# Kernel optimization log

Measured on AMD Instinct MI355X. Metric: run time of the kernel, lower is better.

## Reference

```python
import jax, jax.numpy as jnp
import numpy as np

B, T, OBS = 16, 4095, 128
HID, NH, FF, NL = 256, 8, 1024, 4
DH = HID // NH
ACT = 32
KEPS = 0.001   # performer kernel_epsilon (generalized attention default)
LNEPS = 1e-6   # flax LayerNorm default eps


def setup_inputs() -> dict:
    key = jax.random.key(0)
    ks = list(jax.random.split(key, 16))
    s = 0.02
    r = lambda k, shape: jax.random.normal(k, shape, jnp.float32) * s
    return {
        "hidden_state": jnp.zeros((B, 1, HID), jnp.float32),
        "ins": jax.random.normal(ks[0], (B, T, OBS), jnp.float32),
        "resets": jax.random.randint(ks[1], (B,), 0, 2).astype(bool),
        "emb_W": r(ks[2], (OBS, HID)), "emb_b": jnp.zeros((HID,), jnp.float32),
        "Wq": r(ks[3], (NL, HID, NH, DH)), "bq": jnp.zeros((NL, NH, DH), jnp.float32),
        "Wk": r(ks[4], (NL, HID, NH, DH)), "bk": jnp.zeros((NL, NH, DH), jnp.float32),
        "Wv": r(ks[5], (NL, HID, NH, DH)), "bv": jnp.zeros((NL, NH, DH), jnp.float32),
        "Wo": r(ks[6], (NL, NH, DH, HID)), "bo": jnp.zeros((NL, HID), jnp.float32),
        "ln1_s": jnp.ones((NL, HID), jnp.float32), "ln1_b": jnp.zeros((NL, HID), jnp.float32),
        "W1": r(ks[7], (NL, HID, FF)), "b1": jnp.zeros((NL, FF), jnp.float32),
        "W2": r(ks[8], (NL, FF, HID)), "b2": jnp.zeros((NL, HID), jnp.float32),
        "ln2_s": jnp.ones((NL, HID), jnp.float32), "ln2_b": jnp.zeros((NL, HID), jnp.float32),
        "qp_W": r(ks[9], (HID, ACT)), "qp_b": jnp.zeros((ACT,), jnp.float32),
    }


def layer_norm(x, scale, bias):
    m = x.mean(-1, keepdims=True)
    v = ((x - m) ** 2).mean(-1, keepdims=True)
    return (x - m) * jax.lax.rsqrt(v + LNEPS) * scale + bias


def favor_attention(q, k, v):
    # FAVOR+ generalized attention with deterministic relu features (no random
    # projection, make_fast_generalized_attention defaults), bidirectional,
    # renormalized. q,k,v: [B, L, H, Dh]; feature dim M == Dh.
    qp = jax.nn.relu(q) + KEPS
    kp = jax.nn.relu(k) + KEPS
    kv = jnp.einsum('blhm,blhd->bhmd', kp, v)            # [B,H,M,Dh]
    num = jnp.einsum('blhm,bhmd->blhd', qp, kv)           # [B,L,H,Dh]
    den = jnp.einsum('blhm,bhm->blh', qp, kp.sum(axis=1))  # [B,L,H]
    return num / den[..., None]


def encoder_block(x, Wq, bq, Wk, bk, Wv, bv, Wo, bo, ln1_s, ln1_b, W1, b1, W2, b2, ln2_s, ln2_b):
    q = jnp.einsum('bld,dhm->blhm', x, Wq) + bq
    k = jnp.einsum('bld,dhm->blhm', x, Wk) + bk
    v = jnp.einsum('bld,dhm->blhm', x, Wv) + bv
    a = favor_attention(q, k, v)
    o = jnp.einsum('blhm,hmd->bld', a, Wo) + bo
    x = o + o  # faithful to source: x = attn(x); x = x + dropout(x)
    x = layer_norm(x, ln1_s, ln1_b)
    h = jax.nn.relu(x @ W1 + b1) @ W2 + b2
    h = h + h  # same residual quirk on the FFN branch
    return layer_norm(h, ln2_s, ln2_b)


def reference(hidden_state, ins, resets, emb_W, emb_b, Wq, bq, Wk, bk, Wv, bv, Wo, bo, ln1_s, ln1_b, W1, b1, W2, b2, ln2_s, ln2_b, qp_W, qp_b):
    emb = ins @ emb_W + emb_b                         # [B, T, HID]
    hs = jnp.where(resets[:, None, None], 0.0, hidden_state)
    x = jnp.concatenate([hs, emb], axis=-2)           # [B, 1+T, HID]
    for i in range(NL):
        x = encoder_block(x, Wq[i], bq[i], Wk[i], bk[i], Wv[i], bv[i], Wo[i], bo[i],
                          ln1_s[i], ln1_b[i], W1[i], b1[i], W2[i], b2[i], ln2_s[i], ln2_b[i])
    new_hidden = x[..., 0:1, :]                       # carry token
    q_vals = new_hidden @ qp_W + qp_b                 # [B, 1, ACT]
    return new_hidden, q_vals
```

## Files before the change

### kernel.cpp

```cpp
#include <hip/hip_runtime.h>


typedef unsigned short bf16_t;
typedef __attribute__((ext_vector_type(8))) short short8;
typedef __attribute__((ext_vector_type(4))) float float4v;

#define NB 16
#define LSEQ 4096
#define MROWS (NB * LSEQ)
#define HIDD 256
#define NHEAD 8
#define DHEAD 32
#define FFD 1024
#define NLAY 4
#define KEPS_F 1e-3f
#define LNEPS_F 1e-6f
#define KV_ELEMS (NB * NHEAD * 32 * 33)

__device__ __forceinline__ float b2f(bf16_t h) {
    return __uint_as_float(((unsigned int)h) << 16);
}
__device__ __forceinline__ bf16_t f2b(float f) {
    unsigned int u = __float_as_uint(f);
    u += 0x7fffu + ((u >> 16) & 1u);
    return (bf16_t)(u >> 16);
}

#define GLOAD_LDS16(g, l)                                                     \
    __builtin_amdgcn_global_load_lds(                                         \
        (const __attribute__((address_space(1))) void*)(g),                   \
        (__attribute__((address_space(3))) void*)(l), 16, 0, 0)

#define SBAR() __builtin_amdgcn_s_barrier()
#define WAITV(n)                                                              \
    do {                                                                      \
        asm volatile("s_waitcnt vmcnt(" #n ")" ::: "memory");                 \
        __builtin_amdgcn_sched_barrier(0);                                    \
    } while (0)

#define FRAG16(L, R)                                                          \
    (*(const short8*)&(L)[((((R) >> 1) * 8) +                                  \
        (((((R) & 1) << 2) | quad) ^ (((R) >> 1) & 7))) * 8])

__global__ __launch_bounds__(256) void conv_transpose_kernel(
    const float* __restrict__ in, bf16_t* __restrict__ out, int R, int C,
    size_t ils, size_t ols)
{
    __shared__ float tile[32][33];
    const size_t ib = (size_t)blockIdx.z * ils;
    const size_t ob = (size_t)blockIdx.z * ols;
    const int r0 = blockIdx.y * 32, c0 = blockIdx.x * 32;
    const int tx = threadIdx.x & 31, ty = threadIdx.x >> 5;
#pragma unroll
    for (int rr = ty; rr < 32; rr += 8)
        tile[rr][tx] = in[ib + (size_t)(r0 + rr) * C + c0 + tx];
    __syncthreads();
#pragma unroll
    for (int rr = ty; rr < 32; rr += 8)
        out[ob + (size_t)(c0 + rr) * R + r0 + tx] = f2b(tile[tx][rr]);
}

__global__ __launch_bounds__(256) void concat_bias_kernel(
    const float* __restrict__ bq, const float* __restrict__ bk,
    const float* __restrict__ bv, float* __restrict__ bqkv)
{
    const int l = blockIdx.x, j = threadIdx.x;
    bqkv[l * 768 + j]       = bq[l * 256 + j];
    bqkv[l * 768 + 256 + j] = bk[l * 256 + j];
    bqkv[l * 768 + 512 + j] = bv[l * 256 + j];
}

__global__ __launch_bounds__(256) void prep_a_kernel(
    const float* __restrict__ ins, bf16_t* __restrict__ Ain)
{
    const int row = blockIdx.x * 2 + (threadIdx.x >> 7);
    const int j = threadIdx.x & 127;
    const int b = row >> 12, l = row & (LSEQ - 1);
    bf16_t v = 0;
    if (l != 0) v = f2b(ins[((size_t)b * 4095 + (l - 1)) * 128 + j]);
    Ain[(size_t)row * 128 + j] = v;
}

__global__ __launch_bounds__(256) void fix_row0_kernel(
    const float* __restrict__ hidden, const int* __restrict__ resets,
    bf16_t* __restrict__ X)
{
    const int b = blockIdx.x, j = threadIdx.x;
    float v = resets[b] ? 0.f : hidden[b * HIDD + j];
    X[((size_t)b * LSEQ) * HIDD + j] = f2b(v);
}

template <int MODE>
__global__ __launch_bounds__(512, 2) void gemm_mfma256(
    const bf16_t* __restrict__ A, const bf16_t* __restrict__ WT,
    const float* __restrict__ bias, bf16_t* __restrict__ C,
    int M, int N, int K, int lda, int ldc)
{
    __shared__ __align__(16) bf16_t As[4][256 * 32];
    __shared__ __align__(16) bf16_t Bs[4][256 * 32];

    const int tid = threadIdx.x;
    const int wave = tid >> 6, lane = tid & 63;
    const int quad = lane >> 4, mr = lane & 15;

    const int Nn = N >> 8;
    const int id = blockIdx.x;
    const int s = id >> 3;
    const int bm = (((id & 7) + ((s / Nn) << 3))) << 8;
    const int bn = (s % Nn) << 8;

    const int wm = (wave & 1) << 7;
    const int wn = (wave >> 1) << 6;

    const int KT = K >> 5;

    float bcol[4];
#pragma unroll
    for (int j = 0; j < 4; ++j) bcol[j] = bias[bn + wn + j * 16 + mr];
    asm volatile("s_waitcnt vmcnt(0)" ::: "memory");
    __builtin_amdgcn_sched_barrier(0);

    auto stageA = [&](int t) {
        const int k0 = t << 5;
        bf16_t* L = &As[t & 3][0];
#pragma unroll
        for (int it = 0; it < 2; ++it) {
            const int c = it * 512 + tid;
            const int r = c >> 2;
            const int up = ((((r & 1) << 2) | (c & 3)) ^ ((r >> 1) & 7));
            const int grow = ((r >> 1) << 1) | (up >> 2);
            GLOAD_LDS16(A + (size_t)(bm + grow) * lda + k0 + ((up & 3) << 3),
                        L + c * 8);
        }
    };
    auto stageB = [&](int t) {
        const int k0 = t << 5;
        bf16_t* L = &Bs[t & 3][0];
#pragma unroll
        for (int it = 0; it < 2; ++it) {
            const int c = it * 512 + tid;
            const int r = c >> 2;
            const int up = ((((r & 1) << 2) | (c & 3)) ^ ((r >> 1) & 7));
            const int grow = ((r >> 1) << 1) | (up >> 2);
            GLOAD_LDS16(WT + (size_t)(bn + grow) * K + k0 + ((up & 3) << 3),
                        L + c * 8);
        }
    };

    float4v acc[8][4];
#pragma unroll
    for (int i = 0; i < 8; i++)
#pragma unroll
        for (int j = 0; j < 4; j++) acc[i][j] = (float4v)(0.f);

    const int P = KT < 3 ? KT : 3;
    for (int tt = 0; tt < P; ++tt) { stageA(tt); stageB(tt); }

    for (int t = 0; t < KT; ++t) {
        const int ahead = KT - 1 - t;
        if (ahead >= 2) { WAITV(8); } else if (ahead == 1) { WAITV(4); } else { WAITV(0); }
        SBAR();
        const bf16_t* LA = &As[t & 3][0];
        const bf16_t* LB = &Bs[t & 3][0];
        short8 a[4], b[4];
#pragma unroll
        for (int j = 0; j < 4; ++j) b[j] = FRAG16(LB, wn + j * 16 + mr);
#pragma unroll
        for (int i = 0; i < 4; ++i) a[i] = FRAG16(LA, wm + i * 16 + mr);
        if (t + 3 < KT) stageA(t + 3);
        SBAR();
        __builtin_amdgcn_s_setprio(1);
        __builtin_amdgcn_sched_barrier(0);
#pragma unroll
        for (int i = 0; i < 4; ++i)
#pragma unroll
            for (int j = 0; j < 4; ++j)
                acc[i][j] = __builtin_amdgcn_mfma_f32_16x16x32_bf16(
                    a[i], b[j], acc[i][j], 0, 0, 0);
        __builtin_amdgcn_sched_barrier(0);
        __builtin_amdgcn_s_setprio(0);
        SBAR();
#pragma unroll
        for (int i = 0; i < 4; ++i) a[i] = FRAG16(LA, wm + 64 + i * 16 + mr);
        if (t + 3 < KT) stageB(t + 3);
        SBAR();
        __builtin_amdgcn_s_setprio(1);
        __builtin_amdgcn_sched_barrier(0);
#pragma unroll
        for (int i = 0; i < 4; ++i)
#pragma unroll
            for (int j = 0; j < 4; ++j)
                acc[4 + i][j] = __builtin_amdgcn_mfma_f32_16x16x32_bf16(
                    a[i], b[j], acc[4 + i][j], 0, 0, 0);
        __builtin_amdgcn_sched_barrier(0);
        __builtin_amdgcn_s_setprio(0);
    }

#pragma unroll
    for (int i = 0; i < 8; ++i) {
#pragma unroll
        for (int r = 0; r < 4; ++r) {
            const int grow = bm + wm + i * 16 + quad * 4 + r;
            bf16_t* crow = C + (size_t)grow * ldc + bn + wn + mr;
#pragma unroll
            for (int j = 0; j < 4; ++j) {
                float v = acc[i][j][r] + bcol[j];
                if (MODE == 1) v = fmaxf(v, 0.f);
                crow[j * 16] = f2b(v);
            }
        }
    }
}

__global__ __launch_bounds__(512, 2) void gemm_ln256(
    const bf16_t* __restrict__ A, const bf16_t* __restrict__ WT,
    const float* __restrict__ bias, const float* __restrict__ sc,
    const float* __restrict__ bi, bf16_t* __restrict__ out,
    int K, int lda)
{
    __shared__ __align__(16) bf16_t As[4][256 * 32];
    __shared__ __align__(16) bf16_t Bs[4][256 * 32];
    __shared__ float red[8][128][2];
    __shared__ float fin[256][2];

    const int tid = threadIdx.x;
    const int wave = tid >> 6, lane = tid & 63;
    const int quad = lane >> 4, mr = lane & 15;
    const int bm = blockIdx.x << 8;

    const int wm = (wave & 1) << 7;
    const int wn = (wave >> 1) << 6;

    const int KT = K >> 5;

    float bcol[4], scv[4], biv[4];
#pragma unroll
    for (int j = 0; j < 4; ++j) {
        bcol[j] = bias[wn + j * 16 + mr];
        scv[j]  = sc[wn + j * 16 + mr];
        biv[j]  = bi[wn + j * 16 + mr];
    }
    asm volatile("s_waitcnt vmcnt(0)" ::: "memory");
    __builtin_amdgcn_sched_barrier(0);

    auto stageA = [&](int t) {
        const int k0 = t << 5;
        bf16_t* L = &As[t & 3][0];
#pragma unroll
        for (int it = 0; it < 2; ++it) {
            const int c = it * 512 + tid;
            const int r = c >> 2;
            const int up = ((((r & 1) << 2) | (c & 3)) ^ ((r >> 1) & 7));
            const int grow = ((r >> 1) << 1) | (up >> 2);
            GLOAD_LDS16(A + (size_t)(bm + grow) * lda + k0 + ((up & 3) << 3),
                        L + c * 8);
        }
    };
    auto stageB = [&](int t) {
        const int k0 = t << 5;
        bf16_t* L = &Bs[t & 3][0];
#pragma unroll
        for (int it = 0; it < 2; ++it) {
            const int c = it * 512 + tid;
            const int r = c >> 2;
            const int up = ((((r & 1) << 2) | (c & 3)) ^ ((r >> 1) & 7));
            const int grow = ((r >> 1) << 1) | (up >> 2);
            GLOAD_LDS16(WT + (size_t)grow * K + k0 + ((up & 3) << 3),
                        L + c * 8);
        }
    };

    float4v acc[8][4];
#pragma unroll
    for (int i = 0; i < 8; i++)
#pragma unroll
        for (int j = 0; j < 4; j++) acc[i][j] = (float4v)(0.f);

    const int P = KT < 3 ? KT : 3;
    for (int tt = 0; tt < P; ++tt) { stageA(tt); stageB(tt); }

    for (int t = 0; t < KT; ++t) {
        const int ahead = KT - 1 - t;
        if (ahead >= 2) { WAITV(8); } else if (ahead == 1) { WAITV(4); } else { WAITV(0); }
        SBAR();
        const bf16_t* LA = &As[t & 3][0];
        const bf16_t* LB = &Bs[t & 3][0];
        short8 a[4], b[4];
#pragma unroll
        for (int j = 0; j < 4; ++j) b[j] = FRAG16(LB, wn + j * 16 + mr);
#pragma unroll
        for (int i = 0; i < 4; ++i) a[i] = FRAG16(LA, wm + i * 16 + mr);
        if (t + 3 < KT) stageA(t + 3);
        SBAR();
        __builtin_amdgcn_s_setprio(1);
        __builtin_amdgcn_sched_barrier(0);
#pragma unroll
        for (int i = 0; i < 4; ++i)
#pragma unroll
            for (int j = 0; j < 4; ++j)
                acc[i][j] = __builtin_amdgcn_mfma_f32_16x16x32_bf16(
                    a[i], b[j], acc[i][j], 0, 0, 0);
        __builtin_amdgcn_sched_barrier(0);
        __builtin_amdgcn_s_setprio(0);
        SBAR();
#pragma unroll
        for (int i = 0; i < 4; ++i) a[i] = FRAG16(LA, wm + 64 + i * 16 + mr);
        if (t + 3 < KT) stageB(t + 3);
        SBAR();
        __builtin_amdgcn_s_setprio(1);
        __builtin_amdgcn_sched_barrier(0);
#pragma unroll
        for (int i = 0; i < 4; ++i)
#pragma unroll
            for (int j = 0; j < 4; ++j)
                acc[4 + i][j] = __builtin_amdgcn_mfma_f32_16x16x32_bf16(
                    a[i], b[j], acc[4 + i][j], 0, 0, 0);
        __builtin_amdgcn_sched_barrier(0);
        __builtin_amdgcn_s_setprio(0);
    }

#pragma unroll
    for (int i = 0; i < 8; ++i) {
#pragma unroll
        for (int r = 0; r < 4; ++r) {
            float ss = 0.f, s2 = 0.f;
#pragma unroll
            for (int j = 0; j < 4; ++j) {
                const float v = 2.0f * (acc[i][j][r] + bcol[j]);
                ss += v; s2 += v * v;
            }
#pragma unroll
            for (int off = 1; off < 16; off <<= 1) {
                ss += __shfl_xor(ss, off, 64);
                s2 += __shfl_xor(s2, off, 64);
            }
            if (mr == 0) {
                const int rl = i * 16 + quad * 4 + r;
                red[wave][rl][0] = ss;
                red[wave][rl][1] = s2;
            }
        }
    }
    __syncthreads();
    {
        const int R = tid >> 1, p = tid & 1;
        const int mh = R >> 7, rl = R & 127;
        fin[R][p] = red[mh][rl][p] + red[mh + 2][rl][p]
                  + red[mh + 4][rl][p] + red[mh + 6][rl][p];
    }
    __syncthreads();

#pragma unroll
    for (int i = 0; i < 8; ++i) {
#pragma unroll
        for (int r = 0; r < 4; ++r) {
            const int R = wm + i * 16 + quad * 4 + r;
            const float mean = fin[R][0] * (1.0f / 256.0f);
            const float var  = fin[R][1] * (1.0f / 256.0f) - mean * mean;
            const float rs = rsqrtf(var + LNEPS_F);
            bf16_t* crow = out + (size_t)(bm + R) * 256 + wn + mr;
#pragma unroll
            for (int j = 0; j < 4; ++j) {
                const float v = 2.0f * (acc[i][j][r] + bcol[j]);
                crow[j * 16] = f2b((v - mean) * rs * scv[j] + biv[j]);
            }
        }
    }
}

__global__ __launch_bounds__(512) void gemm_favor_ln_mfma(
    const bf16_t* __restrict__ QKV, const float* __restrict__ KV,
    const bf16_t* __restrict__ WT, const float* __restrict__ bias,
    const float* __restrict__ sc, const float* __restrict__ bi,
    bf16_t* __restrict__ out)
{
    __shared__ __align__(16) bf16_t As[128 * 64];
    __shared__ __align__(16) bf16_t Bs[256 * 64];
    __shared__ __align__(16) bf16_t kvT[NHEAD * 34 * 36];
    __shared__ float red[8][64][2];
    __shared__ float fin[128][2];

    const int tid = threadIdx.x;
    const int wave = tid >> 6, lane = tid & 63;
    const int bm = blockIdx.x * 128;
    const int b = bm >> 12;
    const int quad = lane >> 4, mr = lane & 15;
    const int mxor = mr & 7;
    const int wm0 = (wave & 1) * 64;
    const int wn0 = (wave >> 1) * 64;

    for (int e = tid; e < NHEAD * 34 * 32; e += 512) {
        const int h = e / (34 * 32);
        const int rem = e - h * (34 * 32);
        const int d = rem >> 5, m = rem & 31;
        bf16_t v = 0;
        if (d < 33) v = f2b(KV[((size_t)(b * NHEAD + h)) * (32 * 33) + m * 33 + d]);
        kvT[(h * 34 + d) * 36 + m] = v;
    }
    __syncthreads();

    float4v acc[4][4];
#pragma unroll
    for (int i = 0; i < 4; i++)
#pragma unroll
        for (int j = 0; j < 4; j++) acc[i][j] = (float4v)(0.f);

    for (int k0 = 0; k0 < 256; k0 += 64) {
#pragma unroll
        for (int it = 0; it < 4; it++) {
            const int c = it * 512 + tid;
            const int r = c >> 3;
            const int kofs = ((c & 7) ^ (r & 7)) * 8;
            GLOAD_LDS16(WT + (size_t)r * 256 + k0 + kofs, &Bs[c * 8]);
        }
        const int h0 = k0 >> 5;
        const int Rrow = bm + wave * 16 + mr;
#pragma unroll
        for (int hh = 0; hh < 2; hh++) {
            const int h = h0 + hh;
            short8 araw = *(const short8*)(QKV + (size_t)Rrow * 768 + h * 32 + quad * 8);
            short8 a;
#pragma unroll
            for (int j = 0; j < 8; j++)
                a[j] = (short)f2b(fmaxf(b2f((bf16_t)araw[j]), 0.f) + KEPS_F);
            short8 bf0 = *(const short8*)&kvT[(h * 34 + mr) * 36 + quad * 8];
            short8 bf1 = *(const short8*)&kvT[(h * 34 + 16 + mr) * 36 + quad * 8];
            short8 bden;
#pragma unroll
            for (int j = 0; j < 8; j++) bden[j] = 0;
            if (mr == 0)
                bden = *(const short8*)&kvT[(h * 34 + 32) * 36 + quad * 8];
            float4v c0 = __builtin_amdgcn_mfma_f32_16x16x32_bf16(a, bf0, (float4v)(0.f), 0, 0, 0);
            float4v c1 = __builtin_amdgcn_mfma_f32_16x16x32_bf16(a, bf1, (float4v)(0.f), 0, 0, 0);
            float4v c2 = __builtin_amdgcn_mfma_f32_16x16x32_bf16(a, bden, (float4v)(0.f), 0, 0, 0);
#pragma unroll
            for (int r = 0; r < 4; r++) {
                const float den = __shfl(c2[r], quad << 4);
                const float rinv = 1.0f / den;
                const int R = wave * 16 + quad * 4 + r;
                const int ca = hh * 32 + mr;
                const int cbn = hh * 32 + 16 + mr;
                As[(R * 8 + ((ca >> 3) ^ (R & 7))) * 8 + (ca & 7)]   = f2b(c0[r] * rinv);
                As[(R * 8 + ((cbn >> 3) ^ (R & 7))) * 8 + (cbn & 7)] = f2b(c1[r] * rinv);
            }
        }
        __syncthreads();
#pragma unroll
        for (int kk = 0; kk < 8; kk += 4) {
            short8 a[4], bfr[4];
#pragma unroll
            for (int i = 0; i < 4; i++)
                a[i] = *(const short8*)&As[((wm0 + i * 16 + mr) * 8 + ((quad + kk) ^ mxor)) * 8];
#pragma unroll
            for (int j = 0; j < 4; j++)
                bfr[j] = *(const short8*)&Bs[((wn0 + j * 16 + mr) * 8 + ((quad + kk) ^ mxor)) * 8];
#pragma unroll
            for (int i = 0; i < 4; i++)
#pragma unroll
                for (int j = 0; j < 4; j++)
                    acc[i][j] = __builtin_amdgcn_mfma_f32_16x16x32_bf16(
                        a[i], bfr[j], acc[i][j], 0, 0, 0);
        }
        __syncthreads();
    }

    float bcol[4];
#pragma unroll
    for (int j = 0; j < 4; j++) bcol[j] = bias[wn0 + j * 16 + mr];

#pragma unroll
    for (int i = 0; i < 4; i++) {
#pragma unroll
        for (int r = 0; r < 4; r++) {
            float s = 0.f, s2 = 0.f;
#pragma unroll
            for (int j = 0; j < 4; j++) {
                const float v = 2.0f * (acc[i][j][r] + bcol[j]);
                s += v; s2 += v * v;
            }
#pragma unroll
            for (int off = 1; off < 16; off <<= 1) {
                s  += __shfl_xor(s, off, 64);
                s2 += __shfl_xor(s2, off, 64);
            }
            if (mr == 0) {
                const int rl = i * 16 + quad * 4 + r;
                red[wave][rl][0] = s;
                red[wave][rl][1] = s2;
            }
        }
    }
    __syncthreads();
    if (tid < 256) {
        const int R = tid >> 1, p = tid & 1;
        const int mh = R >> 6, rl = R & 63;
        fin[R][p] = red[mh][rl][p] + red[mh + 2][rl][p]
                  + red[mh + 4][rl][p] + red[mh + 6][rl][p];
    }
    __syncthreads();

    float scv[4], biv[4];
#pragma unroll
    for (int j = 0; j < 4; j++) {
        scv[j] = sc[wn0 + j * 16 + mr];
        biv[j] = bi[wn0 + j * 16 + mr];
    }
#pragma unroll
    for (int i = 0; i < 4; i++) {
#pragma unroll
        for (int r = 0; r < 4; r++) {
            const int R = wm0 + i * 16 + quad * 4 + r;
            const float mean = fin[R][0] * (1.0f / 256.0f);
            const float var  = fin[R][1] * (1.0f / 256.0f) - mean * mean;
            const float rs = rsqrtf(var + LNEPS_F);
            bf16_t* crow = out + (size_t)(bm + R) * 256 + wn0 + mr;
#pragma unroll
            for (int j = 0; j < 4; j++) {
                const float v = 2.0f * (acc[i][j][r] + bcol[j]);
                crow[j * 16] = f2b((v - mean) * rs * scv[j] + biv[j]);
            }
        }
    }
}

__global__ __launch_bounds__(256) void zero_kv(float* __restrict__ KV)
{
    int i = blockIdx.x * 256 + threadIdx.x;
    if (i < KV_ELEMS) KV[i] = 0.f;
}

__global__ __launch_bounds__(256) void kv_mfma(
    const bf16_t* __restrict__ QKV, float* __restrict__ KV)
{
    __shared__ __align__(16) char smem[24576];
    bf16_t (*kp)[36] = (bf16_t(*)[36])smem;
    bf16_t (*vv)[52] = (bf16_t(*)[52])(smem + 9216);
    float (*red)[6][64][4] = (float(*)[6][64][4])smem;

    const int bh = blockIdx.x;
    const int b = bh >> 3, h = bh & 7;
    const size_t rowbase = (size_t)b * LSEQ + blockIdx.y * 512;
    const int tid = threadIdx.x;
    const int wave = tid >> 6, lane = tid & 63;
    const int quad = lane >> 4, mr = lane & 15;

    for (int e = tid; e < 128 * 20; e += 256) {
        const int l = e / 20, c = 32 + (e % 20);
        vv[l][c] = (c == 32) ? (bf16_t)0x3F80 : (bf16_t)0;
    }

    float4v acc[2][3];
#pragma unroll
    for (int i = 0; i < 2; i++)
#pragma unroll
        for (int t = 0; t < 3; t++) acc[i][t] = (float4v)(0.f);

    for (int pass = 0; pass < 4; pass++) {
        __syncthreads();
        const size_t lp = rowbase + pass * 128;
#pragma unroll
        for (int it = 0; it < 4; it++) {
            const int e = tid + it * 256;
            const int l = e >> 3, c0 = (e & 7) * 4;
            const bf16_t* src = QKV + (lp + l) * 768 + 256 + h * 32 + c0;
            ushort4 kq = *(const ushort4*)src;
            ushort4 vq = *(const ushort4*)(src + 256);
            ushort4 ko;
            ko.x = f2b(fmaxf(b2f(kq.x), 0.f) + KEPS_F);
            ko.y = f2b(fmaxf(b2f(kq.y), 0.f) + KEPS_F);
            ko.z = f2b(fmaxf(b2f(kq.z), 0.f) + KEPS_F);
            ko.w = f2b(fmaxf(b2f(kq.w), 0.f) + KEPS_F);
            *(ushort4*)&kp[l][c0] = ko;
            *(ushort4*)&vv[l][c0] = vq;
        }
        __syncthreads();

        const int lw = wave * 32 + quad * 8;
        short8 a[2], bb[3];
#pragma unroll
        for (int i = 0; i < 2; i++)
#pragma unroll
            for (int j = 0; j < 8; j++)
                a[i][j] = (short)kp[lw + j][i * 16 + mr];
#pragma unroll
        for (int t = 0; t < 3; t++)
#pragma unroll
            for (int j = 0; j < 8; j++)
                bb[t][j] = (short)vv[lw + j][t * 16 + mr];
#pragma unroll
        for (int i = 0; i < 2; i++)
#pragma unroll
            for (int t = 0; t < 3; t++)
                acc[i][t] = __builtin_amdgcn_mfma_f32_16x16x32_bf16(
                    a[i], bb[t], acc[i][t], 0, 0, 0);
    }

    __syncthreads();
#pragma unroll
    for (int i = 0; i < 2; i++)
#pragma unroll
        for (int t = 0; t < 3; t++)
#pragma unroll
            for (int r = 0; r < 4; r++)
                red[wave][i * 3 + t][lane][r] = acc[i][t][r];
    __syncthreads();

    float* dst = KV + (size_t)bh * (32 * 33);
    for (int e = tid; e < 6 * 64 * 4; e += 256) {
        const int t = e >> 8, li = (e >> 2) & 63, r = e & 3;
        const float s = red[0][t][li][r] + red[1][t][li][r]
                      + red[2][t][li][r] + red[3][t][li][r];
        const int i = t / 3, j = t % 3;
        const int m = i * 16 + (li >> 4) * 4 + r;
        const int d = j * 16 + (li & 15);
        if (d < 33) atomicAdd(&dst[m * 33 + d], s);
    }
}

__global__ __launch_bounds__(256) void head_kernel(
    const bf16_t* __restrict__ X, const float* __restrict__ qpW,
    const float* __restrict__ qpb, float* __restrict__ out)
{
    const int b = blockIdx.x, j = threadIdx.x;
    __shared__ float xr[HIDD];
    float v = b2f(X[((size_t)b * LSEQ) * HIDD + j]);
    xr[j] = v;
    out[b * HIDD + j] = v;
    __syncthreads();
    if (j < 32) {
        float acc = qpb[j];
        for (int d = 0; d < HIDD; d++)
            acc = fmaf(xr[d], qpW[d * 32 + j], acc);
        out[NB * HIDD + b * 32 + j] = acc;
    }
}

extern "C" void kernel_launch(void* const* d_in, const int* in_sizes, int n_in,
                              void* d_out, int out_size, void* d_ws, size_t ws_size,
                              hipStream_t stream)
{
    const float* hidden = (const float*)d_in[0];
    const float* ins    = (const float*)d_in[1];
    const int*   resets = (const int*)d_in[2];
    const float* embW   = (const float*)d_in[3];
    const float* embb   = (const float*)d_in[4];
    const float* Wq = (const float*)d_in[5];
    const float* bq = (const float*)d_in[6];
    const float* Wk = (const float*)d_in[7];
    const float* bk = (const float*)d_in[8];
    const float* Wv = (const float*)d_in[9];
    const float* bv = (const float*)d_in[10];
    const float* Wo = (const float*)d_in[11];
    const float* bo = (const float*)d_in[12];
    const float* ln1s = (const float*)d_in[13];
    const float* ln1b = (const float*)d_in[14];
    const float* W1 = (const float*)d_in[15];
    const float* b1 = (const float*)d_in[16];
    const float* W2 = (const float*)d_in[17];
    const float* b2 = (const float*)d_in[18];
    const float* ln2s = (const float*)d_in[19];
    const float* ln2b = (const float*)d_in[20];
    const float* qpW = (const float*)d_in[21];
    const float* qpb = (const float*)d_in[22];

    const size_t ACT_SZ = (size_t)MROWS * HIDD;
    bf16_t* X    = (bf16_t*)d_ws;
    bf16_t* QKV  = X + ACT_SZ;
    bf16_t* H1   = QKV;
    bf16_t* Ain  = QKV;
    float*  KV   = (float*)(QKV + (size_t)MROWS * FFD);
    float*  bqkv = KV + KV_ELEMS;
    bf16_t* WqkvT = (bf16_t*)(bqkv + NLAY * 768);
    bf16_t* WoT   = WqkvT + (size_t)NLAY * 3 * HIDD * HIDD;
    bf16_t* W1T   = WoT + (size_t)NLAY * HIDD * HIDD;
    bf16_t* W2T   = W1T + (size_t)NLAY * HIDD * FFD;
    bf16_t* embWT = W2T + (size_t)NLAY * FFD * HIDD;

    const dim3 blk(256);
    const dim3 blk512(512);
    const size_t HH = (size_t)HIDD * HIDD;

    conv_transpose_kernel<<<dim3(8, 8, NLAY), blk, 0, stream>>>(Wq, WqkvT,          HIDD, HIDD, HH, 3 * HH);
    conv_transpose_kernel<<<dim3(8, 8, NLAY), blk, 0, stream>>>(Wk, WqkvT + HH,     HIDD, HIDD, HH, 3 * HH);
    conv_transpose_kernel<<<dim3(8, 8, NLAY), blk, 0, stream>>>(Wv, WqkvT + 2 * HH, HIDD, HIDD, HH, 3 * HH);
    conv_transpose_kernel<<<dim3(8, 8, NLAY), blk, 0, stream>>>(Wo, WoT, HIDD, HIDD, HH, HH);
    conv_transpose_kernel<<<dim3(32, 8, NLAY), blk, 0, stream>>>(W1, W1T, HIDD, FFD, (size_t)HIDD * FFD, (size_t)HIDD * FFD);
    conv_transpose_kernel<<<dim3(8, 32, NLAY), blk, 0, stream>>>(W2, W2T, FFD, HIDD, (size_t)HIDD * FFD, (size_t)HIDD * FFD);
    conv_transpose_kernel<<<dim3(8, 4, 1), blk, 0, stream>>>(embW, embWT, 128, HIDD, 0, 0);
    concat_bias_kernel<<<NLAY, blk, 0, stream>>>(bq, bk, bv, bqkv);

    prep_a_kernel<<<MROWS / 2, blk, 0, stream>>>(ins, Ain);
    gemm_mfma256<0><<<dim3(256), blk512, 0, stream>>>(Ain, embWT, embb, X, MROWS, HIDD, 128, 128, HIDD);
    fix_row0_kernel<<<NB, blk, 0, stream>>>(hidden, resets, X);

    for (int l = 0; l < NLAY; l++) {
        gemm_mfma256<0><<<dim3(256 * 3), blk512, 0, stream>>>(X, WqkvT + (size_t)l * 3 * HH,
                                                              bqkv + l * 768, QKV, MROWS, 768, HIDD, HIDD, 768);

        zero_kv<<<(KV_ELEMS + 255) / 256, blk, 0, stream>>>(KV);
        kv_mfma<<<dim3(NB * NHEAD, 8), blk, 0, stream>>>(QKV, KV);

        gemm_favor_ln_mfma<<<MROWS / 128, blk512, 0, stream>>>(
            QKV, KV, WoT + (size_t)l * HH, bo + l * HIDD,
            ln1s + l * HIDD, ln1b + l * HIDD, X);

        gemm_mfma256<1><<<dim3(256 * 4), blk512, 0, stream>>>(X, W1T + (size_t)l * HIDD * FFD,
                                                              b1 + l * FFD, H1, MROWS, FFD, HIDD, HIDD, FFD);
        gemm_ln256<<<dim3(256), blk512, 0, stream>>>(
            H1, W2T + (size_t)l * FFD * HIDD, b2 + l * HIDD,
            ln2s + l * HIDD, ln2b + l * HIDD, X, FFD, FFD);
    }

    head_kernel<<<NB, blk, 0, stream>>>(X, qpW, qpb, (float*)d_out);
}
```

Before: 1.078 ms.

## Shrink GEMM tiles to 128x256 with single-barrier triple-buffered pipeline

The dense GEMM and GEMM+LayerNorm kernels now use 128-row tiles instead of 256, with accumulators halved and launch bounds raised for higher occupancy. The grids double in size. The K-loop is restructured to a 3-stage LDS ring with prefetch distance two, issued right after one barrier per iteration, replacing the four-buffer scheme with split A/B prefetches and four barriers. The aim is to cut LDS footprint and barrier overhead and to raise occupancy. The cost is less data reuse per tile and more redundant B-tile loads.

```diff
diff --git a/kernel.cpp b/kernel.cpp
--- a/kernel.cpp
+++ b/kernel.cpp
@@ -91,13 +91,13 @@
 }
 
 template <int MODE>
-__global__ __launch_bounds__(512, 2) void gemm_mfma256(
+__global__ __launch_bounds__(512, 4) void gemm_pipe(
     const bf16_t* __restrict__ A, const bf16_t* __restrict__ WT,
     const float* __restrict__ bias, bf16_t* __restrict__ C,
     int M, int N, int K, int lda, int ldc)
 {
-    __shared__ __align__(16) bf16_t As[4][256 * 32];
-    __shared__ __align__(16) bf16_t Bs[4][256 * 32];
+    __shared__ __align__(16) bf16_t As[3][128 * 32];
+    __shared__ __align__(16) bf16_t Bs[3][256 * 32];
 
     const int tid = threadIdx.x;
     const int wave = tid >> 6, lane = tid & 63;
@@ -106,10 +106,10 @@
     const int Nn = N >> 8;
     const int id = blockIdx.x;
     const int s = id >> 3;
-    const int bm = (((id & 7) + ((s / Nn) << 3))) << 8;
+    const int bm = (((id & 7) + ((s / Nn) << 3))) << 7;
     const int bn = (s % Nn) << 8;
 
-    const int wm = (wave & 1) << 7;
+    const int wm = (wave & 1) << 6;
     const int wn = (wave >> 1) << 6;
 
     const int KT = K >> 5;
@@ -122,20 +122,17 @@
 
     auto stageA = [&](int t) {
         const int k0 = t << 5;
-        bf16_t* L = &As[t & 3][0];
-#pragma unroll
-        for (int it = 0; it < 2; ++it) {
-            const int c = it * 512 + tid;
-            const int r = c >> 2;
-            const int up = ((((r & 1) << 2) | (c & 3)) ^ ((r >> 1) & 7));
-            const int grow = ((r >> 1) << 1) | (up >> 2);
-            GLOAD_LDS16(A + (size_t)(bm + grow) * lda + k0 + ((up & 3) << 3),
-                        L + c * 8);
-        }
+        bf16_t* L = &As[t % 3][0];
+        const int c = tid;
+        const int r = c >> 2;
+        const int up = ((((r & 1) << 2) | (c & 3)) ^ ((r >> 1) & 7));
+        const int grow = ((r >> 1) << 1) | (up >> 2);
+        GLOAD_LDS16(A + (size_t)(bm + grow) * lda + k0 + ((up & 3) << 3),
+                    L + c * 8);
     };
     auto stageB = [&](int t) {
         const int k0 = t << 5;
-        bf16_t* L = &Bs[t & 3][0];
+        bf16_t* L = &Bs[t % 3][0];
 #pragma unroll
         for (int it = 0; it < 2; ++it) {
             const int c = it * 512 + tid;
@@ -147,28 +144,27 @@
         }
     };
 
-    float4v acc[8][4];
-#pragma unroll
-    for (int i = 0; i < 8; i++)
+    float4v acc[4][4];
+#pragma unroll
+    for (int i = 0; i < 4; i++)
 #pragma unroll
         for (int j = 0; j < 4; j++) acc[i][j] = (float4v)(0.f);
 
-    const int P = KT < 3 ? KT : 3;
+    const int P = KT < 2 ? KT : 2;
     for (int tt = 0; tt < P; ++tt) { stageA(tt); stageB(tt); }
 
     for (int t = 0; t < KT; ++t) {
-        const int ahead = KT - 1 - t;
-        if (ahead >= 2) { WAITV(8); } else if (ahead == 1) { WAITV(4); } else { WAITV(0); }
+        if (t < KT - 1) { WAITV(3); } else { WAITV(0); }
         SBAR();
-        const bf16_t* LA = &As[t & 3][0];
-        const bf16_t* LB = &Bs[t & 3][0];
+        __builtin_amdgcn_sched_barrier(0);
+        if (t + 2 < KT) { stageA(t + 2); stageB(t + 2); }
+        const bf16_t* LA = &As[t % 3][0];
+        const bf16_t* LB = &Bs[t % 3][0];
         short8 a[4], b[4];
 #pragma unroll
         for (int j = 0; j < 4; ++j) b[j] = FRAG16(LB, wn + j * 16 + mr);
 #pragma unroll
         for (int i = 0; i < 4; ++i) a[i] = FRAG16(LA, wm + i * 16 + mr);
-        if (t + 3 < KT) stageA(t + 3);
-        SBAR();
         __builtin_amdgcn_s_setprio(1);
         __builtin_amdgcn_sched_barrier(0);
 #pragma unroll
@@ -179,25 +175,10 @@
                     a[i], b[j], acc[i][j], 0, 0, 0);
         __builtin_amdgcn_sched_barrier(0);
         __builtin_amdgcn_s_setprio(0);
-        SBAR();
-#pragma unroll
-        for (int i = 0; i < 4; ++i) a[i] = FRAG16(LA, wm + 64 + i * 16 + mr);
-        if (t + 3 < KT) stageB(t + 3);
-        SBAR();
-        __builtin_amdgcn_s_setprio(1);
-        __builtin_amdgcn_sched_barrier(0);
-#pragma unroll
-        for (int i = 0; i < 4; ++i)
-#pragma unroll
-            for (int j = 0; j < 4; ++j)
-                acc[4 + i][j] = __builtin_amdgcn_mfma_f32_16x16x32_bf16(
-                    a[i], b[j], acc[4 + i][j], 0, 0, 0);
-        __builtin_amdgcn_sched_barrier(0);
-        __builtin_amdgcn_s_setprio(0);
-    }
-
-#pragma unroll
-    for (int i = 0; i < 8; ++i) {
+    }
+
+#pragma unroll
+    for (int i = 0; i < 4; ++i) {
 #pragma unroll
         for (int r = 0; r < 4; ++r) {
             const int grow = bm + wm + i * 16 + quad * 4 + r;
@@ -212,23 +193,23 @@
     }
 }
 
-__global__ __launch_bounds__(512, 2) void gemm_ln256(
+__global__ __launch_bounds__(512, 4) void gemm_ln_pipe(
     const bf16_t* __restrict__ A, const bf16_t* __restrict__ WT,
     const float* __restrict__ bias, const float* __restrict__ sc,
     const float* __restrict__ bi, bf16_t* __restrict__ out,
     int K, int lda)
 {
-    __shared__ __align__(16) bf16_t As[4][256 * 32];
-    __shared__ __align__(16) bf16_t Bs[4][256 * 32];
-    __shared__ float red[8][128][2];
-    __shared__ float fin[256][2];
+    __shared__ __align__(16) bf16_t As[3][128 * 32];
+    __shared__ __align__(16) bf16_t Bs[3][256 * 32];
+    __shared__ float red[8][64][2];
+    __shared__ float fin[128][2];
 
     const int tid = threadIdx.x;
     const int wave = tid >> 6, lane = tid & 63;
     const int quad = lane >> 4, mr = lane & 15;
-    const int bm = blockIdx.x << 8;
-
-    const int wm = (wave & 1) << 7;
+    const int bm = blockIdx.x << 7;
+
+    const int wm = (wave & 1) << 6;
     const int wn = (wave >> 1) << 6;
 
     const int KT = K >> 5;
@@ -245,20 +226,17 @@
 
     auto stageA = [&](int t) {
         const int k0 = t << 5;
-        bf16_t* L = &As[t & 3][0];
-#pragma unroll
-        for (int it = 0; it < 2; ++it) {
-            const int c = it * 512 + tid;
-            const int r = c >> 2;
-            const int up = ((((r & 1) << 2) | (c & 3)) ^ ((r >> 1) & 7));
-            const int grow = ((r >> 1) << 1) | (up >> 2);
-            GLOAD_LDS16(A + (size_t)(bm + grow) * lda + k0 + ((up & 3) << 3),
-                        L + c * 8);
-        }
+        bf16_t* L = &As[t % 3][0];
+        const int c = tid;
+        const int r = c >> 2;
+        const int up = ((((r & 1) << 2) | (c & 3)) ^ ((r >> 1) & 7));
+        const int grow = ((r >> 1) << 1) | (up >> 2);
+        GLOAD_LDS16(A + (size_t)(bm + grow) * lda + k0 + ((up & 3) << 3),
+                    L + c * 8);
     };
     auto stageB = [&](int t) {
         const int k0 = t << 5;
-        bf16_t* L = &Bs[t & 3][0];
+        bf16_t* L = &Bs[t % 3][0];
 #pragma unroll
         for (int it = 0; it < 2; ++it) {
             const int c = it * 512 + tid;
@@ -270,28 +248,27 @@
         }
     };
 
-    float4v acc[8][4];
-#pragma unroll
-    for (int i = 0; i < 8; i++)
+    float4v acc[4][4];
+#pragma unroll
+    for (int i = 0; i < 4; i++)
 #pragma unroll
         for (int j = 0; j < 4; j++) acc[i][j] = (float4v)(0.f);
 
-    const int P = KT < 3 ? KT : 3;
+    const int P = KT < 2 ? KT : 2;
     for (int tt = 0; tt < P; ++tt) { stageA(tt); stageB(tt); }
 
     for (int t = 0; t < KT; ++t) {
-        const int ahead = KT - 1 - t;
-        if (ahead >= 2) { WAITV(8); } else if (ahead == 1) { WAITV(4); } else { WAITV(0); }
+        if (t < KT - 1) { WAITV(3); } else { WAITV(0); }
         SBAR();
-        const bf16_t* LA = &As[t & 3][0];
-        const bf16_t* LB = &Bs[t & 3][0];
+        __builtin_amdgcn_sched_barrier(0);
+        if (t + 2 < KT) { stageA(t + 2); stageB(t + 2); }
+        const bf16_t* LA = &As[t % 3][0];
+        const bf16_t* LB = &Bs[t % 3][0];
         short8 a[4], b[4];
 #pragma unroll
         for (int j = 0; j < 4; ++j) b[j] = FRAG16(LB, wn + j * 16 + mr);
 #pragma unroll
         for (int i = 0; i < 4; ++i) a[i] = FRAG16(LA, wm + i * 16 + mr);
-        if (t + 3 < KT) stageA(t + 3);
-        SBAR();
         __builtin_amdgcn_s_setprio(1);
         __builtin_amdgcn_sched_barrier(0);
 #pragma unroll
@@ -302,25 +279,10 @@
                     a[i], b[j], acc[i][j], 0, 0, 0);
         __builtin_amdgcn_sched_barrier(0);
         __builtin_amdgcn_s_setprio(0);
-        SBAR();
-#pragma unroll
-        for (int i = 0; i < 4; ++i) a[i] = FRAG16(LA, wm + 64 + i * 16 + mr);
-        if (t + 3 < KT) stageB(t + 3);
-        SBAR();
-        __builtin_amdgcn_s_setprio(1);
-        __builtin_amdgcn_sched_barrier(0);
-#pragma unroll
-        for (int i = 0; i < 4; ++i)
-#pragma unroll
-            for (int j = 0; j < 4; ++j)
-                acc[4 + i][j] = __builtin_amdgcn_mfma_f32_16x16x32_bf16(
-                    a[i], b[j], acc[4 + i][j], 0, 0, 0);
-        __builtin_amdgcn_sched_barrier(0);
-        __builtin_amdgcn_s_setprio(0);
-    }
-
-#pragma unroll
-    for (int i = 0; i < 8; ++i) {
+    }
+
+#pragma unroll
+    for (int i = 0; i < 4; ++i) {
 #pragma unroll
         for (int r = 0; r < 4; ++r) {
             float ss = 0.f, s2 = 0.f;
@@ -342,16 +304,16 @@
         }
     }
     __syncthreads();
-    {
+    if (tid < 256) {
         const int R = tid >> 1, p = tid & 1;
-        const int mh = R >> 7, rl = R & 127;
+        const int mh = R >> 6, rl = R & 63;
         fin[R][p] = red[mh][rl][p] + red[mh + 2][rl][p]
                   + red[mh + 4][rl][p] + red[mh + 6][rl][p];
     }
     __syncthreads();
 
 #pragma unroll
-    for (int i = 0; i < 8; ++i) {
+    for (int i = 0; i < 4; ++i) {
 #pragma unroll
         for (int r = 0; r < 4; ++r) {
             const int R = wm + i * 16 + quad * 4 + r;
@@ -690,12 +652,12 @@
     concat_bias_kernel<<<NLAY, blk, 0, stream>>>(bq, bk, bv, bqkv);
 
     prep_a_kernel<<<MROWS / 2, blk, 0, stream>>>(ins, Ain);
-    gemm_mfma256<0><<<dim3(256), blk512, 0, stream>>>(Ain, embWT, embb, X, MROWS, HIDD, 128, 128, HIDD);
+    gemm_pipe<0><<<dim3(512), blk512, 0, stream>>>(Ain, embWT, embb, X, MROWS, HIDD, 128, 128, HIDD);
     fix_row0_kernel<<<NB, blk, 0, stream>>>(hidden, resets, X);
 
     for (int l = 0; l < NLAY; l++) {
-        gemm_mfma256<0><<<dim3(256 * 3), blk512, 0, stream>>>(X, WqkvT + (size_t)l * 3 * HH,
-                                                              bqkv + l * 768, QKV, MROWS, 768, HIDD, HIDD, 768);
+        gemm_pipe<0><<<dim3(512 * 3), blk512, 0, stream>>>(X, WqkvT + (size_t)l * 3 * HH,
+                                                           bqkv + l * 768, QKV, MROWS, 768, HIDD, HIDD, 768);
 
         zero_kv<<<(KV_ELEMS + 255) / 256, blk, 0, stream>>>(KV);
         kv_mfma<<<dim3(NB * NHEAD, 8), blk, 0, stream>>>(QKV, KV);
@@ -704,9 +666,9 @@
             QKV, KV, WoT + (size_t)l * HH, bo + l * HIDD,
             ln1s + l * HIDD, ln1b + l * HIDD, X);
 
-        gemm_mfma256<1><<<dim3(256 * 4), blk512, 0, stream>>>(X, W1T + (size_t)l * HIDD * FFD,
-                                                              b1 + l * FFD, H1, MROWS, FFD, HIDD, HIDD, FFD);
-        gemm_ln256<<<dim3(256), blk512, 0, stream>>>(
+        gemm_pipe<1><<<dim3(512 * 4), blk512, 0, stream>>>(X, W1T + (size_t)l * HIDD * FFD,
+                                                           b1 + l * FFD, H1, MROWS, FFD, HIDD, HIDD, FFD);
+        gemm_ln_pipe<<<dim3(512), blk512, 0, stream>>>(
             H1, W2T + (size_t)l * FFD * HIDD, b2 + l * HIDD,
             ln2s + l * HIDD, ln2b + l * HIDD, X, FFD, FFD);
     }
```

Result: faster. 1.008 ms (-6.4%).
